# Performance work log

Measured on AMD Instinct MI355X. Metric: run time of the kernel, lower is better.

## Reference

```python
import jax, jax.numpy as jnp
import numpy as np

N, E, D_IN, HID, OUT, EDIM, L, NT, ET = 50000, 800000, 128, 128, 128, 32, 3, 2, 3
PUMP = 1
LN_EPS = 1e-5


def setup_inputs() -> dict:
    key = jax.random.key(0)
    ks = jax.random.split(key, 12)
    s = 0.05
    x = jax.random.normal(ks[0], (N, D_IN), jnp.float32)
    edge_index = jax.random.randint(ks[1], (2, E), 0, N, dtype=jnp.int64)
    edge_attr = jax.random.normal(ks[2], (E, EDIM), jnp.float32)
    node_type = jax.random.randint(ks[3], (N,), 0, NT, dtype=jnp.int64)
    edge_type = jax.random.randint(ks[4], (E,), 0, ET, dtype=jnp.int64)
    # per-layer HydroConv params
    node_W = jax.random.normal(ks[5], (L, NT, HID, D_IN), jnp.float32) * s   # per-node-type Linear weight
    node_b = jax.random.normal(ks[6], (L, NT, HID), jnp.float32) * s
    edge_W = jax.random.normal(ks[7], (L, ET, 2, EDIM), jnp.float32) * s     # out dim padded to 2; row 1 only used for pump type
    edge_b = jax.random.normal(ks[8], (L, ET, 2), jnp.float32) * s
    emb = jax.random.normal(ks[9], (L, ET, EDIM), jnp.float32) * s           # edge_type_emb per layer
    ln_g = jnp.ones((L, HID), jnp.float32)
    ln_b = jnp.zeros((L, HID), jnp.float32)
    fc_W = jax.random.normal(ks[10], (OUT, HID), jnp.float32) * s
    fc_b = jnp.zeros((OUT,), jnp.float32)
    return dict(x=x, edge_attr=edge_attr, node_W=node_W, node_b=node_b,
                edge_W=edge_W, edge_b=edge_b, emb=emb, ln_g=ln_g, ln_b=ln_b,
                fc_W=fc_W, fc_b=fc_b, edge_index=edge_index,
                node_type=node_type, edge_type=edge_type)


def _hydro_conv(h, edge_index, edge_attr, node_type, edge_type, nW, nb, eW, eb, emb_l):
    src, dst = edge_index[0], edge_index[1]           # x_j = h[src], x_i = h[dst]
    direction = edge_attr[:, -2:-1]                    # [E,1]
    pump = edge_attr[:, -1:]                           # [E,1]
    ea = edge_attr + emb_l[edge_type]                  # [E,EDIM]
    raw = jnp.einsum('ec,toc->eto', ea, eW) + eb       # [E,ET,2]
    raw = jnp.take_along_axis(raw, edge_type[:, None, None], axis=1)[:, 0]  # [E,2] per-edge-type MLP
    gain = jax.nn.softplus(raw[:, :1])                 # [E,1]
    speed = pump * jnp.where(direction > 0, direction, jnp.ones_like(direction))
    is_pump = (edge_type == PUMP)[:, None]
    gain = jnp.where(is_pump, gain * speed, gain)
    bias = jnp.where(is_pump, raw[:, 1:2] * speed, jnp.zeros_like(gain))
    sign = direction * 2.0 - 1.0
    msg = sign * (gain * (h[src] - h[dst]) + bias)     # [E,C]
    aggr = jax.ops.segment_sum(msg, dst, num_segments=N)  # scatter-add to target nodes
    out = jnp.zeros((N, nW.shape[1]), h.dtype)
    for t in range(NT):                                # per-node-type Linear
        ht = aggr @ nW[t].T + nb[t]
        out = jnp.where((node_type == t)[:, None], ht, out)
    return out


def reference(x, edge_attr, node_W, node_b, edge_W, edge_b, emb, ln_g, ln_b,
              fc_W, fc_b, edge_index, node_type, edge_type):
    h = x
    for l in range(L):
        identity = h
        h = _hydro_conv(h, edge_index, edge_attr, node_type, edge_type,
                        node_W[l], node_b[l], edge_W[l], edge_b[l], emb[l])
        h = jax.nn.relu(h)
        mu = jnp.mean(h, axis=-1, keepdims=True)
        var = jnp.mean(jnp.square(h - mu), axis=-1, keepdims=True)
        h = (h - mu) * jax.lax.rsqrt(var + LN_EPS) * ln_g[l] + ln_b[l]
        if identity.shape == h.shape:                  # residual
            h = h + identity
    return h @ fc_W.T + fc_b
```

## Files before the change

kernel.cpp:

```cpp
#include <hip/hip_runtime.h>
#include <math.h>

#define NN 50000
#define EE 800000
#define D 128
#define EDIM 32
#define LL 3
#define NT 2
#define ET 3
#define NB 196
#define NPAD 50080
#define NT16 3130
#define NBLK16 783

typedef _Float16 f16x8 __attribute__((ext_vector_type(8)));
typedef float f32x4 __attribute__((ext_vector_type(4)));

__device__ __forceinline__ void cvt8(const float4 u, const float4 v, f16x8& hi, f16x8& lo) {
    float x[8] = {u.x, u.y, u.z, u.w, v.x, v.y, v.z, v.w};
#pragma unroll
    for (int e = 0; e < 8; e++) {
        _Float16 h = (_Float16)x[e];
        hi[e] = h;
        lo[e] = (_Float16)(x[e] - (float)h);
    }
}

__global__ __launch_bounds__(256) void k_pcount(const int* __restrict__ nt, int* __restrict__ pc) {
    __shared__ int s[256];
    int d = blockIdx.x * 256 + threadIdx.x;
    int ind = 0;
    if (d < NN) ind = (nt[d] == 0) ? 1 : 0x10000;
    s[threadIdx.x] = ind;
    __syncthreads();
    for (int st = 128; st; st >>= 1) {
        if (threadIdx.x < st) s[threadIdx.x] += s[threadIdx.x + st];
        __syncthreads();
    }
    if (threadIdx.x == 0) pc[blockIdx.x] = s[0];
}

__global__ __launch_bounds__(256) void k_pscan(const int* __restrict__ pc, int* __restrict__ po,
                                               int* __restrict__ meta) {
    __shared__ int s[256];
    int t = threadIdx.x;
    int v = (t < NB) ? pc[t] : 0;
    s[t] = v;
    __syncthreads();
    for (int st = 1; st < 256; st <<= 1) {
        int add = (t >= st) ? s[t - st] : 0;
        __syncthreads();
        s[t] += add;
        __syncthreads();
    }
    if (t < NB) po[t] = s[t] - v;
    if (t == 0) {
        int tot = s[255];
        meta[3] = ((tot & 0xffff) + 63) & ~63;
    }
}

__global__ __launch_bounds__(256) void k_passign(const int* __restrict__ nt, const int* __restrict__ po,
                                                 const int* __restrict__ meta,
                                                 int* __restrict__ pos, int* __restrict__ inv) {
    __shared__ int s[256];
    int t = threadIdx.x;
    int d = blockIdx.x * 256 + t;
    int ty = (d < NN) ? nt[d] : -1;
    int ind = (ty == 0) ? 1 : ((ty == 1) ? 0x10000 : 0);
    s[t] = ind;
    __syncthreads();
    for (int st = 1; st < 256; st <<= 1) {
        int add = (t >= st) ? s[t - st] : 0;
        __syncthreads();
        s[t] += add;
        __syncthreads();
    }
    if (d >= NN) return;
    int excl = s[t] - ind;
    int pop = po[blockIdx.x];
    int p;
    if (ty == 0) p = (pop & 0xffff) + (excl & 0xffff);
    else         p = meta[3] + (pop >> 16) + (excl >> 16);
    pos[d] = p;
    inv[p] = d;
}

__global__ __launch_bounds__(256) void k_permx(const float* __restrict__ x, const int* __restrict__ pos,
                                               float* __restrict__ h0) {
    int flat = blockIdx.x * 256 + threadIdx.x;
    if (flat >= NN * 32) return;
    int d = flat >> 5, f4 = flat & 31;
    int p = pos[d];
    ((float4*)h0)[(size_t)p * 32 + f4] = ((const float4*)x)[(size_t)d * 32 + f4];
}

__global__ __launch_bounds__(256) void k_hist(const int* __restrict__ dst, int* __restrict__ deg) {
    int e = blockIdx.x * 256 + threadIdx.x;
    if (e < EE) atomicAdd(&deg[dst[e]], 1);
}

__global__ __launch_bounds__(256) void k_scan_bsum(const int* __restrict__ deg, int* __restrict__ bsum) {
    __shared__ int s[256];
    int t = threadIdx.x;
    int d = blockIdx.x * 256 + t;
    s[t] = (d < NN) ? deg[d] : 0;
    __syncthreads();
    for (int st = 128; st > 0; st >>= 1) {
        if (t < st) s[t] += s[t + st];
        __syncthreads();
    }
    if (t == 0) bsum[blockIdx.x] = s[0];
}

__global__ __launch_bounds__(256) void k_scan_boff(const int* __restrict__ bsum, int* __restrict__ boff) {
    __shared__ int s[256];
    int t = threadIdx.x;
    s[t] = (t < NB) ? bsum[t] : 0;
    __syncthreads();
    for (int st = 1; st < 256; st <<= 1) {
        int add = (t >= st) ? s[t - st] : 0;
        __syncthreads();
        s[t] += add;
        __syncthreads();
    }
    if (t < NB) boff[t] = (t == 0) ? 0 : s[t - 1];
}

__global__ __launch_bounds__(256) void k_scan_offs(const int* __restrict__ deg, const int* __restrict__ boff,
                                                   int* __restrict__ offs, int* __restrict__ cur) {
    __shared__ int s[256];
    int t = threadIdx.x;
    int d = blockIdx.x * 256 + t;
    int v = (d < NN) ? deg[d] : 0;
    s[t] = v;
    __syncthreads();
    for (int st = 1; st < 256; st <<= 1) {
        int add = (t >= st) ? s[t - st] : 0;
        __syncthreads();
        s[t] += add;
        __syncthreads();
    }
    if (d < NN) {
        int excl = s[t] - v + boff[blockIdx.x];
        offs[d] = excl;
        cur[d]  = excl;
    }
}

__global__ __launch_bounds__(256) void k_scateid(const int* __restrict__ dst,
                                                 int* __restrict__ cur, int* __restrict__ eid) {
    int e = blockIdx.x * 256 + threadIdx.x;
    if (e < EE) {
        int d = dst[e];
        int p = atomicAdd(&cur[d], 1);
        eid[p] = e;
    }
}

__global__ __launch_bounds__(256) void k_edge2(const float* __restrict__ edge_attr,
                                               const float* __restrict__ edge_W,
                                               const float* __restrict__ edge_b,
                                               const float* __restrict__ emb,
                                               const int* __restrict__ ei,
                                               const int* __restrict__ etype,
                                               const int* __restrict__ pos,
                                               const int* __restrict__ eid,
                                               float2* __restrict__ spA,
                                               float* __restrict__ sBn) {
    __shared__ float eWl[18 * 33];
    __shared__ float ebd[18];
    int t0 = threadIdx.x;
    for (int i = t0; i < 18 * EDIM; i += 256) eWl[(i >> 5) * 33 + (i & 31)] = edge_W[i];
    __syncthreads();
    if (t0 < 18) {
        int l = t0 / (ET * 2);
        int rem = t0 % (ET * 2);
        int tt = rem / 2;
        float sum = edge_b[t0];
        const float* em = emb + (l * ET + tt) * EDIM;
        const float* w  = eWl + t0 * 33;
        for (int c = 0; c < EDIM; c++) sum += em[c] * w[c];
        ebd[t0] = sum;
    }
    __syncthreads();
    int p = blockIdx.x * 256 + t0;
    if (p >= EE) return;
    int e = eid[p];

    float a[EDIM];
    const float4* ap = (const float4*)(edge_attr + (size_t)e * EDIM);
#pragma unroll
    for (int i = 0; i < EDIM / 4; i++) {
        float4 v = ap[i];
        a[4 * i + 0] = v.x; a[4 * i + 1] = v.y; a[4 * i + 2] = v.z; a[4 * i + 3] = v.w;
    }
    int tt = etype[e];
    float dir  = a[EDIM - 2];
    float pump = a[EDIM - 1];
    float sign = dir * 2.f - 1.f;
    float speed = pump * (dir > 0.f ? dir : 1.f);
    int src = ei[e];
    int sp = pos[src];
    float Av[LL], Bv[LL];
#pragma unroll
    for (int l = 0; l < LL; l++) {
        const float* w0 = eWl + ((l * ET + tt) * 2 + 0) * 33;
        const float* w1 = w0 + 33;
        float r0 = ebd[(l * ET + tt) * 2 + 0];
        float r1 = ebd[(l * ET + tt) * 2 + 1];
#pragma unroll
        for (int c = 0; c < EDIM; c++) { r0 += a[c] * w0[c]; r1 += a[c] * w1[c]; }
        float gain = fmaxf(r0, 0.f) + log1pf(expf(-fabsf(r0)));
        float bias = 0.f;
        if (tt == 1) { gain *= speed; bias = r1 * speed; }
        Av[l] = sign * gain;
        Bv[l] = sign * bias;
    }
#pragma unroll
    for (int l = 0; l < LL; l++)
        spA[(size_t)l * EE + p] = make_float2(__int_as_float(sp), Av[l]);
    if (tt == 1) {
        int dst = ei[EE + e];
        int pd = pos[dst];
#pragma unroll
        for (int l = 0; l < LL; l++) atomicAdd(&sBn[l * NPAD + pd], Bv[l]);
    }
}

__global__ __launch_bounds__(256) void k_gather(const float* __restrict__ h,
                                                const int* __restrict__ offs,
                                                const int* __restrict__ deg,
                                                const int* __restrict__ pos,
                                                const float2* __restrict__ spA,
                                                const float* __restrict__ sBn,
                                                int layer,
                                                float* __restrict__ aggr) {
    __shared__ float4 rbuf[2][32];
    __shared__ float  rsum[2];
    int local = threadIdx.x;
    int nb = local >> 7;
    int node = blockIdx.x * 2 + nb;
    int t = local & 127;
    int w = t >> 5;
    int f4 = t & 31;
    int start = offs[node];
    int n = deg[node];
    int p = pos[node];
    const float2* sp_l = spA + (size_t)layer * EE;

    float4 acc = make_float4(0.f, 0.f, 0.f, 0.f);
    float sA = 0.f;
    for (int k = w; k < n; k += 8) {
        int k2 = k + 4;
        float2 sa = sp_l[start + k];
        float2 sb = (k2 < n) ? sp_l[start + k2] : make_float2(__int_as_float(0), 0.f);
        int s1 = __float_as_int(sa.x);
        int s2 = __float_as_int(sb.x);
        float4 h1 = *(const float4*)&h[(size_t)s1 * D + 4 * f4];
        float4 h2 = *(const float4*)&h[(size_t)s2 * D + 4 * f4];
        acc.x += sa.y * h1.x + sb.y * h2.x;
        acc.y += sa.y * h1.y + sb.y * h2.y;
        acc.z += sa.y * h1.z + sb.y * h2.z;
        acc.w += sa.y * h1.w + sb.y * h2.w;
        sA += sa.y + sb.y;
    }
    acc.x += __shfl_xor(acc.x, 32); acc.y += __shfl_xor(acc.y, 32);
    acc.z += __shfl_xor(acc.z, 32); acc.w += __shfl_xor(acc.w, 32);
    sA += __shfl_xor(sA, 32);
    if (((local >> 6) & 1) == 1 && (t & 63) < 32) {
        rbuf[nb][f4] = acc;
        if (f4 == 0) rsum[nb] = sA;
    }
    __syncthreads();
    if (((local >> 6) & 1) == 0 && (t & 63) < 32) {
        float4 o = rbuf[nb][f4];
        float sAt = sA + rsum[nb];
        float sBt = sBn[layer * NPAD + p];
        float4 hd = *(const float4*)&h[(size_t)p * D + 4 * f4];
        float4 r;
        r.x = acc.x + o.x - sAt * hd.x + sBt;
        r.y = acc.y + o.y - sAt * hd.y + sBt;
        r.z = acc.z + o.z - sAt * hd.z + sBt;
        r.w = acc.w + o.w - sAt * hd.w + sBt;
        *(float4*)&aggr[(size_t)p * D + 4 * f4] = r;
    }
}

__global__ __launch_bounds__(256) void k_node(const float* __restrict__ aggr,
                                              const float* __restrict__ hprev,
                                              const float* __restrict__ Wg,
                                              const float* __restrict__ bg,
                                              const float* __restrict__ lng,
                                              const float* __restrict__ lnb,
                                              const int* __restrict__ meta,
                                              float* __restrict__ hnext) {
    int wid  = threadIdx.x >> 6;
    int lane = threadIdx.x & 63;
    int w0 = (blockIdx.x * 4 + wid) * 16;
    if (w0 >= NPAD) return;
    int l15 = lane & 15, lg = lane >> 4;
    int tt = (w0 >= meta[3]) ? 1 : 0;
    const float* W = Wg + (size_t)tt * D * D;

    f32x4 acc[8];
#pragma unroll
    for (int j = 0; j < 8; j++) acc[j] = (f32x4){0.f, 0.f, 0.f, 0.f};

#pragma unroll 1
    for (int ks = 0; ks < 4; ks++) {
        int kb = ks * 32 + 8 * lg;
        float4 rA[2], rB[8][2];
        {
            const float* pa = aggr + (size_t)(w0 + l15) * D + kb;
            rA[0] = *(const float4*)pa;
            rA[1] = *(const float4*)(pa + 4);
        }
#pragma unroll
        for (int j = 0; j < 8; j++) {
            const float* pb = W + (size_t)(16 * j + l15) * D + kb;
            rB[j][0] = *(const float4*)pb;
            rB[j][1] = *(const float4*)(pb + 4);
        }
        f16x8 ahi, alo;
        cvt8(rA[0], rA[1], ahi, alo);
#pragma unroll
        for (int j = 0; j < 8; j++) {
            f16x8 bhi, blo;
            cvt8(rB[j][0], rB[j][1], bhi, blo);
            acc[j] = __builtin_amdgcn_mfma_f32_16x16x32_f16(ahi, bhi, acc[j], 0, 0, 0);
            acc[j] = __builtin_amdgcn_mfma_f32_16x16x32_f16(alo, bhi, acc[j], 0, 0, 0);
            acc[j] = __builtin_amdgcn_mfma_f32_16x16x32_f16(ahi, blo, acc[j], 0, 0, 0);
        }
    }

    float bv[8], gv[8], bb[8];
#pragma unroll
    for (int j = 0; j < 8; j++) {
        int col = 16 * j + l15;
        bv[j] = bg[tt * D + col];
        gv[j] = lng[col];
        bb[j] = lnb[col];
    }
#pragma unroll
    for (int j = 0; j < 8; j++)
#pragma unroll
        for (int r = 0; r < 4; r++)
            acc[j][r] = fmaxf(acc[j][r] + bv[j], 0.f);

    float mu[4], rs[4];
#pragma unroll
    for (int r = 0; r < 4; r++) {
        float s = 0.f, s2 = 0.f;
#pragma unroll
        for (int j = 0; j < 8; j++) { float v = acc[j][r]; s += v; s2 += v * v; }
#pragma unroll
        for (int m = 1; m < 16; m <<= 1) { s += __shfl_xor(s, m); s2 += __shfl_xor(s2, m); }
        float mm = s * (1.f / 128.f);
        mu[r] = mm;
        rs[r] = rsqrtf(s2 * (1.f / 128.f) - mm * mm + 1e-5f);
    }

#pragma unroll
    for (int r = 0; r < 4; r++) {
        int row = w0 + 4 * lg + r;
#pragma unroll
        for (int j = 0; j < 8; j++) {
            int col = 16 * j + l15;
            float v = (acc[j][r] - mu[r]) * rs[r] * gv[j] + bb[j]
                      + hprev[(size_t)row * D + col];
            hnext[(size_t)row * D + col] = v;
        }
    }
}

__global__ __launch_bounds__(256) void k_fc(const float* __restrict__ hin,
                                            const float* __restrict__ W,
                                            const float* __restrict__ bias,
                                            const int* __restrict__ inv,
                                            float* __restrict__ out) {
    int wid  = threadIdx.x >> 6;
    int lane = threadIdx.x & 63;
    int w0 = (blockIdx.x * 4 + wid) * 16;
    if (w0 >= NPAD) return;
    int l15 = lane & 15, lg = lane >> 4;

    f32x4 acc[8];
#pragma unroll
    for (int j = 0; j < 8; j++) acc[j] = (f32x4){0.f, 0.f, 0.f, 0.f};

#pragma unroll 1
    for (int ks = 0; ks < 4; ks++) {
        int kb = ks * 32 + 8 * lg;
        float4 rA[2], rB[8][2];
        {
            const float* pa = hin + (size_t)(w0 + l15) * D + kb;
            rA[0] = *(const float4*)pa;
            rA[1] = *(const float4*)(pa + 4);
        }
#pragma unroll
        for (int j = 0; j < 8; j++) {
            const float* pb = W + (size_t)(16 * j + l15) * D + kb;
            rB[j][0] = *(const float4*)pb;
            rB[j][1] = *(const float4*)(pb + 4);
        }
        f16x8 ahi, alo;
        cvt8(rA[0], rA[1], ahi, alo);
#pragma unroll
        for (int j = 0; j < 8; j++) {
            f16x8 bhi, blo;
            cvt8(rB[j][0], rB[j][1], bhi, blo);
            acc[j] = __builtin_amdgcn_mfma_f32_16x16x32_f16(ahi, bhi, acc[j], 0, 0, 0);
            acc[j] = __builtin_amdgcn_mfma_f32_16x16x32_f16(alo, bhi, acc[j], 0, 0, 0);
            acc[j] = __builtin_amdgcn_mfma_f32_16x16x32_f16(ahi, blo, acc[j], 0, 0, 0);
        }
    }

    float bv[8];
#pragma unroll
    for (int j = 0; j < 8; j++) bv[j] = bias[16 * j + l15];

#pragma unroll
    for (int r = 0; r < 4; r++) {
        int row = w0 + 4 * lg + r;
        int orig = inv[row];
        if (orig >= 0) {
#pragma unroll
            for (int j = 0; j < 8; j++)
                out[(size_t)orig * D + 16 * j + l15] = acc[j][r] + bv[j];
        }
    }
}

extern "C" void kernel_launch(void* const* d_in, const int* in_sizes, int n_in,
                              void* d_out, int out_size, void* d_ws, size_t ws_size,
                              hipStream_t stream) {
    const float* x         = (const float*)d_in[0];
    const float* edge_attr = (const float*)d_in[1];
    const float* node_W    = (const float*)d_in[2];
    const float* node_b    = (const float*)d_in[3];
    const float* edge_W    = (const float*)d_in[4];
    const float* edge_b    = (const float*)d_in[5];
    const float* emb       = (const float*)d_in[6];
    const float* ln_g      = (const float*)d_in[7];
    const float* ln_b      = (const float*)d_in[8];
    const float* fc_W      = (const float*)d_in[9];
    const float* fc_b      = (const float*)d_in[10];
    const int*   edge_index = (const int*)d_in[11];
    const int*   node_type  = (const int*)d_in[12];
    const int*   edge_type  = (const int*)d_in[13];
    float* out = (float*)d_out;

    char* w = (char*)d_ws;
    auto alloc = [&](size_t bytes) {
        void* p = (void*)w;
        w += (bytes + 255) & ~(size_t)255;
        return p;
    };
    float*  P     = (float*)alloc((size_t)NPAD * D * 4);
    float*  Q     = (float*)alloc((size_t)NPAD * D * 4);
    float*  G     = (float*)alloc((size_t)NPAD * D * 4);
    float2* spA   = (float2*)alloc((size_t)LL * EE * 8);
    float*  sBn   = (float*)alloc((size_t)LL * NPAD * 4);
    int*    eid   = (int*)alloc((size_t)EE * 4);
    int*    pos   = (int*)alloc((size_t)NN * 4);
    int*    inv   = (int*)alloc((size_t)NPAD * 4);
    int*    deg   = (int*)alloc((size_t)NN * 4);
    int*    offs  = (int*)alloc((size_t)NN * 4);
    int*    cur   = (int*)alloc((size_t)NN * 4);
    int*    bsum  = (int*)alloc(256 * 4);
    int*    boff  = (int*)alloc(256 * 4);
    int*    pc    = (int*)alloc(256 * 4);
    int*    po    = (int*)alloc(256 * 4);
    int*    meta  = (int*)alloc(8 * 4);

    hipMemsetAsync(deg, 0, (size_t)NN * 4, stream);
    hipMemsetAsync(inv, 0xFF, (size_t)NPAD * 4, stream);
    hipMemsetAsync(sBn, 0, (size_t)LL * NPAD * 4, stream);

    k_pcount<<<NB, 256, 0, stream>>>(node_type, pc);
    k_pscan<<<1, 256, 0, stream>>>(pc, po, meta);
    k_passign<<<NB, 256, 0, stream>>>(node_type, po, meta, pos, inv);
    k_permx<<<(NN * 32 + 255) / 256, 256, 0, stream>>>(x, pos, P);

    k_hist<<<(EE + 255) / 256, 256, 0, stream>>>(edge_index + EE, deg);
    k_scan_bsum<<<NB, 256, 0, stream>>>(deg, bsum);
    k_scan_boff<<<1, 256, 0, stream>>>(bsum, boff);
    k_scan_offs<<<NB, 256, 0, stream>>>(deg, boff, offs, cur);
    k_scateid<<<(EE + 255) / 256, 256, 0, stream>>>(edge_index + EE, cur, eid);
    k_edge2<<<(EE + 255) / 256, 256, 0, stream>>>(edge_attr, edge_W, edge_b, emb,
                                                  edge_index, edge_type, pos, eid, spA, sBn);

    const float* hin = P;
    float* outs[LL] = {Q, P, Q};
    for (int l = 0; l < LL; l++) {
        k_gather<<<NN / 2, 256, 0, stream>>>(hin, offs, deg, pos, spA, sBn, l, G);
        k_node<<<NBLK16, 256, 0, stream>>>(G, hin,
                                           node_W + (size_t)l * NT * D * D,
                                           node_b + (size_t)l * NT * D,
                                           ln_g + (size_t)l * D,
                                           ln_b + (size_t)l * D,
                                           meta, outs[l]);
        hin = outs[l];
    }
    k_fc<<<NBLK16, 256, 0, stream>>>(hin, fc_W, fc_b, inv, out);
}
```

Measured before the change: 675.5 us.

## Fuse edge scatter into edge MLP and pack per-edge coefficients for all layers

The separate edge-id scatter kernel is merged into the edge MLP kernel, which now reads edges in original order and scatters its results straight to CSR positions via atomicAdd on the cursor. All three layers' gain and bias coefficients plus the source position go into a 32-byte packed record per edge. The per-node bias atomics and their memset are removed, and the bias is summed inside the gather instead. The cost is that each gather now reads 32 bytes per edge instead of 8, and it does this three times, once per layer.

New measurement: 623.0 us. 7.8% less time.

```diff
diff --git a/kernel.cpp b/kernel.cpp
--- a/kernel.cpp
+++ b/kernel.cpp
@@ -148,26 +148,15 @@
     }
 }
 
-__global__ __launch_bounds__(256) void k_scateid(const int* __restrict__ dst,
-                                                 int* __restrict__ cur, int* __restrict__ eid) {
-    int e = blockIdx.x * 256 + threadIdx.x;
-    if (e < EE) {
-        int d = dst[e];
-        int p = atomicAdd(&cur[d], 1);
-        eid[p] = e;
-    }
-}
-
-__global__ __launch_bounds__(256) void k_edge2(const float* __restrict__ edge_attr,
-                                               const float* __restrict__ edge_W,
-                                               const float* __restrict__ edge_b,
-                                               const float* __restrict__ emb,
-                                               const int* __restrict__ ei,
-                                               const int* __restrict__ etype,
-                                               const int* __restrict__ pos,
-                                               const int* __restrict__ eid,
-                                               float2* __restrict__ spA,
-                                               float* __restrict__ sBn) {
+__global__ __launch_bounds__(256) void k_edge(const float* __restrict__ edge_attr,
+                                              const float* __restrict__ edge_W,
+                                              const float* __restrict__ edge_b,
+                                              const float* __restrict__ emb,
+                                              const int* __restrict__ ei,
+                                              const int* __restrict__ etype,
+                                              const int* __restrict__ pos,
+                                              int* __restrict__ cur,
+                                              float4* __restrict__ esort) {
     __shared__ float eWl[18 * 33];
     __shared__ float ebd[18];
     int t0 = threadIdx.x;
@@ -179,14 +168,13 @@
         int tt = rem / 2;
         float sum = edge_b[t0];
         const float* em = emb + (l * ET + tt) * EDIM;
-        const float* w  = eWl + t0 * 33;
-        for (int c = 0; c < EDIM; c++) sum += em[c] * w[c];
+        const float* wq  = eWl + t0 * 33;
+        for (int c = 0; c < EDIM; c++) sum += em[c] * wq[c];
         ebd[t0] = sum;
     }
     __syncthreads();
-    int p = blockIdx.x * 256 + t0;
-    if (p >= EE) return;
-    int e = eid[p];
+    int e = blockIdx.x * 256 + t0;
+    if (e >= EE) return;
 
     float a[EDIM];
     const float4* ap = (const float4*)(edge_attr + (size_t)e * EDIM);
@@ -201,7 +189,9 @@
     float sign = dir * 2.f - 1.f;
     float speed = pump * (dir > 0.f ? dir : 1.f);
     int src = ei[e];
+    int dst = ei[EE + e];
     int sp = pos[src];
+    int p = atomicAdd(&cur[dst], 1);
     float Av[LL], Bv[LL];
 #pragma unroll
     for (int l = 0; l < LL; l++) {
@@ -217,27 +207,21 @@
         Av[l] = sign * gain;
         Bv[l] = sign * bias;
     }
-#pragma unroll
-    for (int l = 0; l < LL; l++)
-        spA[(size_t)l * EE + p] = make_float2(__int_as_float(sp), Av[l]);
-    if (tt == 1) {
-        int dst = ei[EE + e];
-        int pd = pos[dst];
-#pragma unroll
-        for (int l = 0; l < LL; l++) atomicAdd(&sBn[l * NPAD + pd], Bv[l]);
-    }
+    float4 e0 = make_float4(__int_as_float(sp), Av[0], Av[1], Av[2]);
+    float4 e1 = make_float4(Bv[0], Bv[1], Bv[2], 0.f);
+    esort[(size_t)p * 2 + 0] = e0;
+    esort[(size_t)p * 2 + 1] = e1;
 }
 
 __global__ __launch_bounds__(256) void k_gather(const float* __restrict__ h,
                                                 const int* __restrict__ offs,
                                                 const int* __restrict__ deg,
                                                 const int* __restrict__ pos,
-                                                const float2* __restrict__ spA,
-                                                const float* __restrict__ sBn,
+                                                const float4* __restrict__ esort,
                                                 int layer,
                                                 float* __restrict__ aggr) {
     __shared__ float4 rbuf[2][32];
-    __shared__ float  rsum[2];
+    __shared__ float  rsum[2][2];
     int local = threadIdx.x;
     int nb = local >> 7;
     int node = blockIdx.x * 2 + nb;
@@ -247,36 +231,45 @@
     int start = offs[node];
     int n = deg[node];
     int p = pos[node];
-    const float2* sp_l = spA + (size_t)layer * EE;
 
     float4 acc = make_float4(0.f, 0.f, 0.f, 0.f);
-    float sA = 0.f;
+    float sA = 0.f, sB = 0.f;
     for (int k = w; k < n; k += 8) {
         int k2 = k + 4;
-        float2 sa = sp_l[start + k];
-        float2 sb = (k2 < n) ? sp_l[start + k2] : make_float2(__int_as_float(0), 0.f);
-        int s1 = __float_as_int(sa.x);
-        int s2 = __float_as_int(sb.x);
+        bool ok2 = (k2 < n);
+        size_t i1 = (size_t)(start + k) * 2;
+        size_t i2 = ok2 ? (size_t)(start + k2) * 2 : i1;
+        float4 e0 = esort[i1];
+        float4 e1 = esort[i1 + 1];
+        float4 f0 = esort[i2];
+        float4 f1 = esort[i2 + 1];
+        int s1 = __float_as_int(e0.x);
+        int s2 = __float_as_int(f0.x);
         float4 h1 = *(const float4*)&h[(size_t)s1 * D + 4 * f4];
         float4 h2 = *(const float4*)&h[(size_t)s2 * D + 4 * f4];
-        acc.x += sa.y * h1.x + sb.y * h2.x;
-        acc.y += sa.y * h1.y + sb.y * h2.y;
-        acc.z += sa.y * h1.z + sb.y * h2.z;
-        acc.w += sa.y * h1.w + sb.y * h2.w;
-        sA += sa.y + sb.y;
+        float A1 = (layer == 0) ? e0.y : ((layer == 1) ? e0.z : e0.w);
+        float B1 = (layer == 0) ? e1.x : ((layer == 1) ? e1.y : e1.z);
+        float A2 = (layer == 0) ? f0.y : ((layer == 1) ? f0.z : f0.w);
+        float B2 = (layer == 0) ? f1.x : ((layer == 1) ? f1.y : f1.z);
+        if (!ok2) { A2 = 0.f; B2 = 0.f; }
+        acc.x += A1 * h1.x + A2 * h2.x;
+        acc.y += A1 * h1.y + A2 * h2.y;
+        acc.z += A1 * h1.z + A2 * h2.z;
+        acc.w += A1 * h1.w + A2 * h2.w;
+        sA += A1 + A2; sB += B1 + B2;
     }
     acc.x += __shfl_xor(acc.x, 32); acc.y += __shfl_xor(acc.y, 32);
     acc.z += __shfl_xor(acc.z, 32); acc.w += __shfl_xor(acc.w, 32);
-    sA += __shfl_xor(sA, 32);
+    sA += __shfl_xor(sA, 32); sB += __shfl_xor(sB, 32);
     if (((local >> 6) & 1) == 1 && (t & 63) < 32) {
         rbuf[nb][f4] = acc;
-        if (f4 == 0) rsum[nb] = sA;
+        if (f4 == 0) { rsum[nb][0] = sA; rsum[nb][1] = sB; }
     }
     __syncthreads();
     if (((local >> 6) & 1) == 0 && (t & 63) < 32) {
         float4 o = rbuf[nb][f4];
-        float sAt = sA + rsum[nb];
-        float sBt = sBn[layer * NPAD + p];
+        float sAt = sA + rsum[nb][0];
+        float sBt = sB + rsum[nb][1];
         float4 hd = *(const float4*)&h[(size_t)p * D + 4 * f4];
         float4 r;
         r.x = acc.x + o.x - sAt * hd.x + sBt;
@@ -460,9 +453,7 @@
     float*  P     = (float*)alloc((size_t)NPAD * D * 4);
     float*  Q     = (float*)alloc((size_t)NPAD * D * 4);
     float*  G     = (float*)alloc((size_t)NPAD * D * 4);
-    float2* spA   = (float2*)alloc((size_t)LL * EE * 8);
-    float*  sBn   = (float*)alloc((size_t)LL * NPAD * 4);
-    int*    eid   = (int*)alloc((size_t)EE * 4);
+    float4* esort = (float4*)alloc((size_t)EE * 32);
     int*    pos   = (int*)alloc((size_t)NN * 4);
     int*    inv   = (int*)alloc((size_t)NPAD * 4);
     int*    deg   = (int*)alloc((size_t)NN * 4);
@@ -476,7 +467,6 @@
 
     hipMemsetAsync(deg, 0, (size_t)NN * 4, stream);
     hipMemsetAsync(inv, 0xFF, (size_t)NPAD * 4, stream);
-    hipMemsetAsync(sBn, 0, (size_t)LL * NPAD * 4, stream);
 
     k_pcount<<<NB, 256, 0, stream>>>(node_type, pc);
     k_pscan<<<1, 256, 0, stream>>>(pc, po, meta);
@@ -487,14 +477,13 @@
     k_scan_bsum<<<NB, 256, 0, stream>>>(deg, bsum);
     k_scan_boff<<<1, 256, 0, stream>>>(bsum, boff);
     k_scan_offs<<<NB, 256, 0, stream>>>(deg, boff, offs, cur);
-    k_scateid<<<(EE + 255) / 256, 256, 0, stream>>>(edge_index + EE, cur, eid);
-    k_edge2<<<(EE + 255) / 256, 256, 0, stream>>>(edge_attr, edge_W, edge_b, emb,
-                                                  edge_index, edge_type, pos, eid, spA, sBn);
+    k_edge<<<(EE + 255) / 256, 256, 0, stream>>>(edge_attr, edge_W, edge_b, emb,
+                                                 edge_index, edge_type, pos, cur, esort);
 
     const float* hin = P;
     float* outs[LL] = {Q, P, Q};
     for (int l = 0; l < LL; l++) {
-        k_gather<<<NN / 2, 256, 0, stream>>>(hin, offs, deg, pos, spA, sBn, l, G);
+        k_gather<<<NN / 2, 256, 0, stream>>>(hin, offs, deg, pos, esort, l, G);
         k_node<<<NBLK16, 256, 0, stream>>>(G, hin,
                                            node_W + (size_t)l * NT * D * D,
                                            node_b + (size_t)l * NT * D,
```
